# Optimization experiments

Measured on AMD Instinct MI355X. Metric: run time of the kernel, lower is better.

## Reference

```python
import jax, jax.numpy as jnp
import numpy as np

B, N, C = 4, 2048, 81
IMG_W, IMG_H = 1024.0, 800.0
SCORE_THRESH = 0.05
NMS_THRESH = 0.5
DETS_PER_IMG = 100
BBOX_XFORM_CLIP = float(np.log(1000.0 / 16.0))
WX, WY, WW, WH = 10.0, 10.0, 5.0, 5.0


def _make_boxes(key, n):
    k1, k2, k3, k4 = jax.random.split(key, 4)
    x1 = jax.random.uniform(k1, (n,)) * (IMG_W - 60.0)
    y1 = jax.random.uniform(k2, (n,)) * (IMG_H - 60.0)
    w = 10.0 + jax.random.uniform(k3, (n,)) * 300.0
    h = 10.0 + jax.random.uniform(k4, (n,)) * 300.0
    return jnp.stack([x1, y1, jnp.minimum(x1 + w, IMG_W - 1.0), jnp.minimum(y1 + h, IMG_H - 1.0)], axis=-1)


def setup_inputs() -> dict:
    key = jax.random.key(0)
    k1, k2, k3, k4 = jax.random.split(key, 4)
    return {
        "class_logits": jax.random.normal(k1, (B * N, C), jnp.float32),
        "box_regression": jax.random.normal(k2, (B * N, C * 8), jnp.float32) * 0.5,
        "left_proposals": _make_boxes(k3, B * N),
        "right_proposals": _make_boxes(k4, B * N),
    }


def decode(rel, boxes):
    widths = boxes[:, 2] - boxes[:, 0] + 1.0
    heights = boxes[:, 3] - boxes[:, 1] + 1.0
    ctr_x = boxes[:, 0] + 0.5 * widths
    ctr_y = boxes[:, 1] + 0.5 * heights
    dx = rel[:, 0::4] / WX
    dy = rel[:, 1::4] / WY
    dw = jnp.minimum(rel[:, 2::4] / WW, BBOX_XFORM_CLIP)
    dh = jnp.minimum(rel[:, 3::4] / WH, BBOX_XFORM_CLIP)
    pcx = dx * widths[:, None] + ctr_x[:, None]
    pcy = dy * heights[:, None] + ctr_y[:, None]
    pw = jnp.exp(dw) * widths[:, None]
    ph = jnp.exp(dh) * heights[:, None]
    x1 = pcx - 0.5 * pw
    y1 = pcy - 0.5 * ph
    x2 = pcx + 0.5 * pw - 1.0
    y2 = pcy + 0.5 * ph - 1.0
    return jnp.stack([x1, y1, x2, y2], axis=-1)  # [M, C, 4]


def clip_boxes(b):
    x1 = jnp.clip(b[..., 0], 0.0, IMG_W - 1.0)
    y1 = jnp.clip(b[..., 1], 0.0, IMG_H - 1.0)
    x2 = jnp.clip(b[..., 2], 0.0, IMG_W - 1.0)
    y2 = jnp.clip(b[..., 3], 0.0, IMG_H - 1.0)
    return jnp.stack([x1, y1, x2, y2], axis=-1)


def pairwise_iou(b):
    area = jnp.clip(b[:, 2] - b[:, 0] + 1.0, 0.0) * jnp.clip(b[:, 3] - b[:, 1] + 1.0, 0.0)
    lt = jnp.maximum(b[:, None, :2], b[None, :, :2])
    rb = jnp.minimum(b[:, None, 2:], b[None, :, 2:])
    wh = jnp.clip(rb - lt + 1.0, 0.0)
    inter = wh[..., 0] * wh[..., 1]
    return inter / jnp.maximum(area[:, None] + area[None, :] - inter, 1e-6)


def nms_keep(boxes, scores):
    # greedy NMS -> boolean keep mask (fixed shape)
    n = scores.shape[0]
    order = jnp.argsort(-scores)
    iou = pairwise_iou(boxes[order])
    idx = jnp.arange(n)
    def body(i, keep):
        sup = (iou[i] > NMS_THRESH) & keep[i] & (idx > i)
        return keep & (~sup)
    keep = jax.lax.fori_loop(0, n, body, jnp.ones((n,), bool))
    return jnp.zeros((n,), bool).at[order].set(keep)


def _per_image(prob, lb, rb):
    # prob [N,C], lb/rb [N,C,4]
    labels = jnp.argmax(prob, axis=-1)
    ar = jnp.arange(prob.shape[0])
    score = prob[ar, labels]
    lbox = lb[ar, labels]
    rbox = rb[ar, labels]
    valid = (labels >= 1) & (score > SCORE_THRESH)
    s = jnp.where(valid, score, -jnp.inf)
    keep = nms_keep(lbox, s) & nms_keep(rbox, s) & valid
    ms = jnp.where(keep, score, -jnp.inf)
    kth = jax.lax.top_k(ms, DETS_PER_IMG)[0][-1]
    keep = keep & (ms >= kth)
    return lbox, rbox, score, keep


def reference(class_logits, box_regression, left_proposals, right_proposals):
    prob = jax.nn.softmax(class_logits, axis=-1)  # [B*N, C]
    reg = box_regression.reshape(-1, C, 8)
    lb = clip_boxes(decode(reg[:, :, :4].reshape(-1, C * 4), left_proposals))
    rb = clip_boxes(decode(reg[:, :, 4:].reshape(-1, C * 4), right_proposals))
    prob = prob.reshape(B, N, C)
    lb = lb.reshape(B, N, C, 4)
    rb = rb.reshape(B, N, C, 4)
    lbox, rbox, score, keep = jax.vmap(_per_image)(prob, lb, rb)
    m = keep[..., None].astype(score.dtype)
    out = jnp.concatenate([lbox * m, rbox * m, jnp.where(keep, score, 0.0)[..., None]], axis=-1)
    return out  # [B, N, 9]
```

## Files before the change

kernel.cpp:

```cpp
#include <hip/hip_runtime.h>
#include <math.h>

#define NPROP 2048
#define NIMG 4
#define NCLS 81
#define REGW 648
#define SCORE_THRESH 0.05f
#define NMS_T 0.5f
#define DETS 100
#define XC 1023.0f
#define YC 799.0f
#define BBOX_CLIP 4.135166556742356f
#define HBIN 128
#define HOFF 2048
#define SEL 320
#define MAXC 512
#define WRD 8
#define TRIP 2560

typedef unsigned long long u64;

__device__ __forceinline__ float areaf(float4 v) {
  return fmaxf(v.z - v.x + 1.0f, 0.0f) * fmaxf(v.w - v.y + 1.0f, 0.0f);
}
__device__ __forceinline__ bool iou_gt(float4 a, float aa, float4 b, float ba) {
  float ix1 = fmaxf(a.x, b.x), iy1 = fmaxf(a.y, b.y);
  float ix2 = fminf(a.z, b.z), iy2 = fminf(a.w, b.w);
  float iw = fmaxf(ix2 - ix1 + 1.0f, 0.0f);
  float ih = fmaxf(iy2 - iy1 + 1.0f, 0.0f);
  float inter = iw * ih;
  return inter > NMS_T * fmaxf(aa + ba - inter, 1e-6f);
}
__device__ __forceinline__ float score_from_v(unsigned v) {
  unsigned uu = ~v;
  unsigned bits = (uu & 0x80000000u) ? (uu & 0x7fffffffu) : ~uu;
  return __uint_as_float(bits);
}
__device__ __forceinline__ float4 decode_side(const float* __restrict__ reg,
                                              const float4* __restrict__ props,
                                              int grow, int ci, int isR) {
  const float* r = reg + (size_t)grow * REGW + ci * 8 + isR * 4;
  float4 P = props[grow];
  float w  = P.z - P.x + 1.0f;
  float h  = P.w - P.y + 1.0f;
  float cx = P.x + 0.5f * w;
  float cy = P.y + 0.5f * h;
  float dx = r[0] / 10.0f;
  float dy = r[1] / 10.0f;
  float dw = fminf(r[2] / 5.0f, BBOX_CLIP);
  float dh = fminf(r[3] / 5.0f, BBOX_CLIP);
  float pcx = dx * w + cx;
  float pcy = dy * h + cy;
  float pw = expf(dw) * w;
  float ph = expf(dh) * h;
  float4 o;
  o.x = fminf(fmaxf(pcx - 0.5f * pw, 0.0f), XC);
  o.y = fminf(fmaxf(pcy - 0.5f * ph, 0.0f), YC);
  o.z = fminf(fmaxf(pcx + 0.5f * pw - 1.0f, 0.0f), XC);
  o.w = fminf(fmaxf(pcy + 0.5f * ph - 1.0f, 0.0f), YC);
  return o;
}

__global__ __launch_bounds__(256) void score_kernel(
    const float* __restrict__ logits, const float* __restrict__ reg,
    const float* __restrict__ lp, const float* __restrict__ rp,
    unsigned* __restrict__ v32G, unsigned short* __restrict__ ci16G,
    float4* __restrict__ bxAllL, float4* __restrict__ bxAllR,
    int* __restrict__ doneG, float* __restrict__ out) {
  int row  = blockIdx.x * 4 + (threadIdx.x >> 6);
  int lane = threadIdx.x & 63;
  if (blockIdx.x < 72) {
    int g = blockIdx.x * 256 + threadIdx.x;
    ((float4*)out)[g] = make_float4(0.f, 0.f, 0.f, 0.f);
  }
  if (blockIdx.x == 100 && threadIdx.x < NIMG) doneG[threadIdx.x] = 0;
  const float* lr = logits + (size_t)row * NCLS;
  float a = lr[lane];
  float b = (lane < NCLS - 64) ? lr[lane + 64] : -INFINITY;
  float v; int ci;
  if (b > a) { v = b; ci = lane + 64; } else { v = a; ci = lane; }
  for (int o = 32; o; o >>= 1) {
    float ov = __shfl_xor(v, o);
    int   oc = __shfl_xor(ci, o);
    if (ov > v || (ov == v && oc < ci)) { v = ov; ci = oc; }
  }
  float e = expf(a - v) + ((lane < NCLS - 64) ? expf(b - v) : 0.0f);
  for (int o = 32; o; o >>= 1) e += __shfl_xor(e, o);
  if (lane == 0) {
    float score = 1.0f / e;
    unsigned vv = 0xFFFFFFFFu;
    if (ci >= 1 && score > SCORE_THRESH) {
      unsigned uu = __float_as_uint(score);
      uu = (uu & 0x80000000u) ? ~uu : (uu | 0x80000000u);
      vv = ~uu;
    }
    v32G[row]  = vv;
    ci16G[row] = (unsigned short)ci;
    bxAllL[row] = decode_side(reg, (const float4*)lp, row, ci, 0);
    bxAllR[row] = decode_side(reg, (const float4*)rp, row, ci, 1);
  }
}

struct SN {
  u64 keys[NPROP];
  unsigned short sidx[NPROP];
  unsigned v32s[NPROP];
  float4 bxL[MAXC], bxR[MAXC];
  float  arL[MAXC], arR[MAXC];
  u64 keepbL[NPROP / 64], keepbR[NPROP / 64];
  u64 rowmL[64], rowmR[64];
  float4 cbL[64], cbR[64];
  float  cbLa[64], cbRa[64];
  u64 aL, aR;
  int cnt, prevCount, done, ccL, ccR, needFB;
  unsigned kthV;
};

__device__ __forceinline__ float4 get_sboxN(SN* S, const float* reg,
                                            const float4* lp4, const float4* rp4,
                                            const unsigned short* ci16G,
                                            int b, int pos, int isR) {
  if (pos < MAXC) return isR ? S->bxR[pos] : S->bxL[pos];
  int row = S->sidx[pos];
  int grow = b * NPROP + row;
  return decode_side(reg, isR ? rp4 : lp4, grow, ci16G[grow], isR);
}

__global__ __launch_bounds__(1024) void nms_finale_kernel(
    const unsigned* __restrict__ v32G, const unsigned short* __restrict__ ci16G,
    const float* __restrict__ reg, const float* __restrict__ lp,
    const float* __restrict__ rp,
    const float4* __restrict__ bxAllL, const float4* __restrict__ bxAllR,
    unsigned short* __restrict__ srowG, unsigned* __restrict__ svG,
    float4* __restrict__ bxLG, float4* __restrict__ bxRG,
    u64* __restrict__ keepLG, u64* __restrict__ keepRG,
    int* __restrict__ doneG, float* __restrict__ out) {
  __shared__ int hist[HBIN];
  __shared__ u64 keys[MAXC];
  __shared__ unsigned short ssort[MAXC];
  __shared__ float4 bx[MAXC];
  __shared__ u64 mat[TRIP];
  __shared__ int Ts, cnts, nv_sh;
  __shared__ SN S;
  int b = blockIdx.x >> 1, side = blockIdx.x & 1;
  int tid = threadIdx.x, ln = tid & 63, w = tid >> 6;
  const unsigned* v32 = v32G + b * NPROP;
  float* ob = out + (size_t)b * NPROP * 9;

  if (tid == 0) { Ts = HBIN - 1; cnts = 0; }
  if (tid < HBIN) hist[tid] = 0;
  __syncthreads();
  for (int p = tid; p < NPROP; p += 1024) {
    unsigned v = v32[p];
    if (v != 0xFFFFFFFFu) {
      int bin = min(max((int)(v >> 19) - HOFF, 0), HBIN - 1);
      atomicAdd(&hist[bin], 1);
    }
  }
  __syncthreads();
  if (w == 0) {
    int b0 = hist[2 * ln], b1 = hist[2 * ln + 1];
    int s = b0 + b1;
    int incl = s;
#pragma unroll
    for (int o = 1; o < 64; o <<= 1) { int n = __shfl_up(incl, o); if (ln >= o) incl += n; }
    int off = incl - s;
    int c0 = off + b0, c1 = off + s;
    if      (c0 >= SEL && off < SEL) Ts = 2 * ln;
    else if (c1 >= SEL && c0  < SEL) Ts = 2 * ln + 1;
    if (ln == 63) nv_sh = incl;
  }
  __syncthreads();
  int T = Ts, nvTot = nv_sh;
  for (int p = tid; p < NPROP; p += 1024) {
    unsigned v = v32[p];
    bool cand = false;
    if (v != 0xFFFFFFFFu) {
      int bin = min(max((int)(v >> 19) - HOFF, 0), HBIN - 1);
      cand = (bin <= T);
    }
    u64 mb = __ballot(cand);
    int lpos = (int)__popcll(mb & ((1ull << ln) - 1ull));
    int wb = 0;
    if (ln == 0 && mb) wb = atomicAdd(&cnts, (int)__popcll(mb));
    wb = __shfl(wb, 0);
    if (cand) {
      int dst = wb + lpos;
      if (dst < MAXC) keys[dst] = ((u64)v << 16) | (unsigned)p;
    }
  }
  __syncthreads();
  int C1 = cnts;
  bool okfast = (C1 <= MAXC);
  int C1f = okfast ? C1 : 0;

  if (okfast && C1 > 0) {
    if (tid < 256) {
      int i0 = tid, i1 = tid + 256;
      u64 k0 = (i0 < C1) ? keys[i0] : ~0ull;
      u64 k1 = (i1 < C1) ? keys[i1] : ~0ull;
      int r0 = 0, r1 = 0;
#pragma unroll 4
      for (int j = 0; j < C1; ++j) {
        u64 kj = keys[j];
        r0 += (kj < k0) ? 1 : 0;
        r1 += (kj < k1) ? 1 : 0;
      }
      if (i0 < C1) {
        unsigned short rw = (unsigned short)(k0 & 0xFFFFull);
        ssort[r0] = rw; srowG[b * MAXC + r0] = rw;
        svG[b * MAXC + r0] = (unsigned)(k0 >> 16);
      }
      if (i1 < C1) {
        unsigned short rw = (unsigned short)(k1 & 0xFFFFull);
        ssort[r1] = rw; srowG[b * MAXC + r1] = rw;
        svG[b * MAXC + r1] = (unsigned)(k1 >> 16);
      }
    }
    __syncthreads();
    if (tid < MAXC) {
      float4 B = make_float4(0.f, 0.f, 0.f, 0.f);
      if (tid < C1) {
        int row = ssort[tid];
        B = (side ? bxAllR : bxAllL)[b * NPROP + row];
        (side ? bxRG : bxLG)[b * MAXC + tid] = B;
      }
      bx[tid] = B;
    }
    __syncthreads();
    int WRDu = (C1 + 63) >> 6;
    {
      int rb = w & 7, part = w >> 3;
      int r = rb * 64 + ln;
      float4 rbx = bx[r];
      float  rar = areaf(rbx);
      int tb = 0;
      for (int k = 0; k < rb; ++k) tb += ((8 - k) | 1);
      int Sw = (8 - rb) | 1;
      u64* myrow = &mat[tb * 64 + ln * Sw];
      for (int cw = rb + part; cw < WRDu; cw += 2) {
        u64 m = 0;
        const float4* cp = &bx[cw * 64];
#pragma unroll 8
        for (int c = 0; c < 64; ++c) {
          float4 cb = cp[c];
          float car = areaf(cb);
          if (iou_gt(rbx, rar, cb, car)) m |= (1ull << c);
        }
        if (cw == rb) m &= ~((2ull << ln) - 1ull);
        myrow[cw - rb] = m;
      }
    }
    __syncthreads();
    if (w == 0) {
      u64 A[WRD];
#pragma unroll
      for (int t = 0; t < WRD; ++t) {
        int b0 = t * 64;
        A[t] = (C1 >= b0 + 64) ? ~0ull : (C1 > b0 ? ((1ull << (C1 - b0)) - 1ull) : 0ull);
      }
      int tbase = 0;
#pragma unroll
      for (int wb = 0; wb < WRD; ++wb) {
        if (wb * 64 < C1) {
          const int Sw = (8 - wb) | 1;
          const u64* rowp = &mat[tbase];
          u64 aw = A[wb];
#pragma unroll
          for (int g = 0; g < 4; ++g) {
            u64 d[16];
#pragma unroll
            for (int k = 0; k < 16; ++k) d[k] = rowp[(g * 16 + k) * Sw];
#pragma unroll
            for (int k = 0; k < 16; ++k) {
              u64 msk = 0ull - ((aw >> (g * 16 + k)) & 1ull);
              aw &= ~(msk & d[k]);
            }
          }
          A[wb] = aw;
          bool alive = (aw >> ln) & 1ull;
#pragma unroll
          for (int t = wb + 1; t < WRD; ++t) {
            if (t * 64 < C1) {
              u64 x = alive ? rowp[ln * Sw + (t - wb)] : 0ull;
#pragma unroll
              for (int o = 1; o < 64; o <<= 1)
                x |= __shfl_xor((unsigned long long)x, o);
              A[t] &= ~x;
            }
          }
        }
        tbase += 64 * ((8 - wb) | 1);
      }
      if (ln == 0) {
        u64* kG = (side ? keepRG : keepLG) + b * WRD;
#pragma unroll
        for (int t = 0; t < WRD; ++t)
          if (t * 64 < C1) kG[t] = A[t];
      }
    }
  }
  __threadfence();
  __syncthreads();
  if (tid == 0) atomicAdd(doneG + b, 1);
  if (side == 1) return;

  if (tid == 0) {
    while (__hip_atomic_load(doneG + b, __ATOMIC_ACQUIRE, __HIP_MEMORY_SCOPE_AGENT) < 2)
      __builtin_amdgcn_s_sleep(8);
  }
  __syncthreads();
  __threadfence();

  if (w == 0) {
    int before = 0;
    unsigned kth = 0;
    for (int wb = 0; wb * 64 < C1f; ++wb) {
      u64 m = keepLG[b * WRD + wb] & keepRG[b * WRD + wb];
      int pos = wb * 64 + ln;
      bool bit = (m >> ln) & 1ull;
      int rank = before + (int)__popcll(m & ((1ull << ln) - 1ull));
      unsigned vA = svG[b * MAXC + pos];
      u64 selm = __ballot(bit && rank == DETS - 1);
      if (selm) kth = __shfl(vA, __ffsll(selm) - 1);
      bool qual = bit && (rank < DETS || vA == kth);
      if (qual) {
        int row = srowG[b * MAXC + pos];
        float4 L = bxLG[b * MAXC + pos], R = bxRG[b * MAXC + pos];
        float* orow = ob + row * 9;
        orow[0]=L.x; orow[1]=L.y; orow[2]=L.z; orow[3]=L.w;
        orow[4]=R.x; orow[5]=R.y; orow[6]=R.z; orow[7]=R.w;
        orow[8]=score_from_v(vA);
      }
      before += (int)__popcll(m);
    }
    if (ln == 0) {
      S.needFB = (before < DETS && nvTot > C1f) ? 1 : 0;
      S.cnt = 0; S.prevCount = 0; S.done = 0; S.kthV = 0u;
    }
  }
  __syncthreads();
  if (!S.needFB) return;

  const float4* lp4 = (const float4*)lp;
  const float4* rp4 = (const float4*)rp;
  float4* ob4 = (float4*)ob;
  float4 z4 = make_float4(0.f, 0.f, 0.f, 0.f);
  for (int i = tid; i < NPROP * 9 / 4; i += 1024) ob4[i] = z4;
  for (int p = tid; p < NPROP; p += 1024) {
    unsigned v = v32G[b * NPROP + p];
    S.v32s[p] = v;
    bool cand = (v != 0xFFFFFFFFu);
    u64 mb = __ballot(cand);
    int lpos = (int)__popcll(mb & ((1ull << ln) - 1ull));
    int wb = 0;
    if (ln == 0 && mb) wb = atomicAdd(&S.cnt, (int)__popcll(mb));
    wb = __shfl(wb, 0);
    if (cand) S.keys[wb + lpos] = ((u64)v << 16) | (unsigned)p;
  }
  __syncthreads();
  int C2 = S.cnt;
  int CbEnd = (C2 + 63) & ~63;
  {
    int i0 = tid, i1 = tid + 1024;
    u64 k0 = (i0 < C2) ? S.keys[i0] : ~0ull;
    u64 k1 = (i1 < C2) ? S.keys[i1] : ~0ull;
    int r0 = 0, r1 = 0;
#pragma unroll 4
    for (int j = 0; j < C2; ++j) {
      u64 kj = S.keys[j];
      r0 += (kj < k0) ? 1 : 0;
      r1 += (kj < k1) ? 1 : 0;
    }
    if (i0 < C2) S.sidx[r0] = (unsigned short)(k0 & 0xFFFFull);
    if (i1 < C2) S.sidx[r1] = (unsigned short)(k1 & 0xFFFFull);
  }
  for (int i = C2 + tid; i < CbEnd; i += 1024) S.sidx[i] = 0;
  for (int wd = tid; wd < NPROP / 64; wd += 1024) {
    int b0 = wd << 6;
    u64 mf = 0ull;
    if (C2 >= b0 + 64) mf = ~0ull;
    else if (C2 > b0)  mf = (1ull << (C2 - b0)) - 1ull;
    S.keepbL[wd] = mf; S.keepbR[wd] = mf;
  }
  __syncthreads();
  {
    int lim = min(CbEnd, MAXC);
    for (int i = tid; i < lim; i += 1024) {
      if (i < C2) {
        int row = S.sidx[i];
        int grow = b * NPROP + row;
        int ci = ci16G[grow];
        float4 L = decode_side(reg, lp4, grow, ci, 0);
        float4 R = decode_side(reg, rp4, grow, ci, 1);
        S.bxL[i] = L; S.arL[i] = areaf(L);
        S.bxR[i] = R; S.arR[i] = areaf(R);
      } else {
        S.bxL[i] = z4; S.arL[i] = 1.0f;
        S.bxR[i] = z4; S.arR[i] = 1.0f;
      }
    }
  }
  __syncthreads();
  for (int base = 0; base < CbEnd; base += 64) {
    {
      int isR = (w >= 8);
      float4 cbx = get_sboxN(&S, reg, lp4, rp4, ci16G, b, base + ln, isR);
      float car = (base + ln < MAXC) ? (isR ? S.arR[base + ln] : S.arL[base + ln])
                                     : areaf(cbx);
      int w8 = w & 7;
#pragma unroll
      for (int k = 0; k < 8; ++k) {
        int row = w8 * 8 + k;
        float4 rbx;
        rbx.x = __shfl(cbx.x, row); rbx.y = __shfl(cbx.y, row);
        rbx.z = __shfl(cbx.z, row); rbx.w = __shfl(cbx.w, row);
        float rar = __shfl(car, row);
        bool bit = (ln > row) && iou_gt(rbx, rar, cbx, car);
        u64 bal = __ballot(bit);
        if (ln == 0) { if (isR) S.rowmR[row] = bal; else S.rowmL[row] = bal; }
      }
    }
    __syncthreads();
    if (tid < 128) {
      int isR = (tid >= 64);
      u64* km = isR ? S.keepbR : S.keepbL;
      u64* rm = isR ? S.rowmR  : S.rowmL;
      u64 a = km[base >> 6];
#pragma unroll
      for (int j = 0; j < 64; ++j)
        a &= ~((0ull - ((a >> j) & 1ull)) & rm[j]);
      if (ln == 0) {
        km[base >> 6] = a;
        if (isR) { S.aR = a; S.ccR = __popcll(a); }
        else     { S.aL = a; S.ccL = __popcll(a); }
      }
      if ((a >> ln) & 1ull) {
        int pos = __popcll(a & ((1ull << ln) - 1ull));
        float4 v = get_sboxN(&S, reg, lp4, rp4, ci16G, b, base + ln, isR);
        if (isR) { S.cbR[pos] = v; S.cbRa[pos] = areaf(v); }
        else     { S.cbL[pos] = v; S.cbLa[pos] = areaf(v); }
      }
    }
    __syncthreads();
    if (w == 0) {
      u64 m = S.aL & S.aR;
      int before = S.prevCount;
      bool bit = (m >> ln) & 1ull;
      int rank = before + (int)__popcll(m & ((1ull << ln) - 1ull));
      int row = S.sidx[base + ln];
      unsigned vA = S.v32s[row];
      u64 selm = __ballot(bit && rank == DETS - 1);
      unsigned keffV = S.kthV;
      if (selm) keffV = __shfl(vA, __ffsll(selm) - 1);
      bool qual = bit && (rank < DETS || vA == keffV);
      if (qual) {
        float4 L = get_sboxN(&S, reg, lp4, rp4, ci16G, b, base + ln, 0);
        float4 R = get_sboxN(&S, reg, lp4, rp4, ci16G, b, base + ln, 1);
        float s = score_from_v(vA);
        float* orow = ob + row * 9;
        orow[0]=L.x; orow[1]=L.y; orow[2]=L.z; orow[3]=L.w;
        orow[4]=R.x; orow[5]=R.y; orow[6]=R.z; orow[7]=R.w;
        orow[8]=s;
      }
      if (ln == 0) {
        if (selm) S.kthV = keffV;
        int nc = before + (int)__popcll(m);
        S.prevCount = nc;
        if (nc >= DETS) {
          int nxt = base + 64;
          bool cont = false;
          if (nxt < C2) cont = (S.v32s[S.sidx[nxt]] == keffV);
          if (!cont) S.done = 1;
        }
      }
    } else {
      int cL = S.ccL, cR = S.ccR;
      if ((cL | cR) != 0) {
        for (int p = base + 64 + (tid - 64); p < CbEnd; p += 960) {
          float4 mbL = get_sboxN(&S, reg, lp4, rp4, ci16G, b, p, 0);
          float al = (p < MAXC) ? S.arL[p] : areaf(mbL);
          bool supL = false;
          for (int q = 0; q < cL; ++q)
            supL = supL || iou_gt(mbL, al, S.cbL[q], S.cbLa[q]);
          if (supL) atomicAnd(&S.keepbL[p >> 6], ~(1ull << (p & 63)));
          float4 mbR = get_sboxN(&S, reg, lp4, rp4, ci16G, b, p, 1);
          float ar_ = (p < MAXC) ? S.arR[p] : areaf(mbR);
          bool supR = false;
          for (int q = 0; q < cR; ++q)
            supR = supR || iou_gt(mbR, ar_, S.cbR[q], S.cbRa[q]);
          if (supR) atomicAnd(&S.keepbR[p >> 6], ~(1ull << (p & 63)));
        }
      }
    }
    __syncthreads();
    if (S.done) break;
  }
}

extern "C" void kernel_launch(void* const* d_in, const int* in_sizes, int n_in,
                              void* d_out, int out_size, void* d_ws, size_t ws_size,
                              hipStream_t stream) {
  const float* logits = (const float*)d_in[0];
  const float* reg    = (const float*)d_in[1];
  const float* lprop  = (const float*)d_in[2];
  const float* rprop  = (const float*)d_in[3];
  float* out = (float*)d_out;

  char* ws = (char*)d_ws;
  unsigned*       v32G   = (unsigned*)(ws + 0);
  unsigned short* ci16G  = (unsigned short*)(ws + 32768);
  unsigned short* srowG  = (unsigned short*)(ws + 49152);
  unsigned*       svG    = (unsigned*)(ws + 53248);
  float4*         bxLG   = (float4*)(ws + 61440);
  float4*         bxRG   = (float4*)(ws + 94208);
  u64*            keepLG = (u64*)(ws + 126976);
  u64*            keepRG = (u64*)(ws + 127232);
  int*            doneG  = (int*)(ws + 127488);
  float4*         bxAllL = (float4*)(ws + 131072);
  float4*         bxAllR = (float4*)(ws + 262144);

  score_kernel<<<NIMG * NPROP / 4, 256,  0, stream>>>(logits, reg, lprop, rprop,
                                                      v32G, ci16G, bxAllL, bxAllR,
                                                      doneG, out);
  nms_finale_kernel<<<2 * NIMG,    1024, 0, stream>>>(v32G, ci16G, reg, lprop, rprop,
                                                      bxAllL, bxAllR, srowG, svG,
                                                      bxLG, bxRG, keepLG, keepRG,
                                                      doneG, out);
}
```

Baseline: 128.5 us.

## Split fused NMS/finale kernel into separate launches instead of spin-wait

Replaces the single NMS+finale kernel, which used a global done-counter with a spin-wait between the left and right side blocks, with two kernels. One runs the per-side NMS and writes counts and flags, the other does the merge, the output writes and the fallback. This removes the inter-block busy-wait and its threadfence, and it also removes the side-1 blocks idling. The cost is one extra kernel launch and a pass of metadata through global memory.

```diff
diff --git a/kernel.cpp b/kernel.cpp
--- a/kernel.cpp
+++ b/kernel.cpp
@@ -66,14 +66,13 @@
     const float* __restrict__ lp, const float* __restrict__ rp,
     unsigned* __restrict__ v32G, unsigned short* __restrict__ ci16G,
     float4* __restrict__ bxAllL, float4* __restrict__ bxAllR,
-    int* __restrict__ doneG, float* __restrict__ out) {
+    float* __restrict__ out) {
   int row  = blockIdx.x * 4 + (threadIdx.x >> 6);
   int lane = threadIdx.x & 63;
   if (blockIdx.x < 72) {
     int g = blockIdx.x * 256 + threadIdx.x;
     ((float4*)out)[g] = make_float4(0.f, 0.f, 0.f, 0.f);
   }
-  if (blockIdx.x == 100 && threadIdx.x < NIMG) doneG[threadIdx.x] = 0;
   const float* lr = logits + (size_t)row * NCLS;
   float a = lr[lane];
   float b = (lane < NCLS - 64) ? lr[lane + 64] : -INFINITY;
@@ -98,6 +97,182 @@
     ci16G[row] = (unsigned short)ci;
     bxAllL[row] = decode_side(reg, (const float4*)lp, row, ci, 0);
     bxAllR[row] = decode_side(reg, (const float4*)rp, row, ci, 1);
+  }
+}
+
+__global__ __launch_bounds__(1024) void nms8_kernel(
+    const unsigned* __restrict__ v32G,
+    const float4* __restrict__ bxAllL, const float4* __restrict__ bxAllR,
+    unsigned short* __restrict__ srowG, unsigned* __restrict__ svG,
+    float4* __restrict__ bxLG, float4* __restrict__ bxRG,
+    u64* __restrict__ keepLG, u64* __restrict__ keepRG,
+    int* __restrict__ C1G, int* __restrict__ C2G, int* __restrict__ flagG) {
+  __shared__ int hist[HBIN];
+  __shared__ u64 keys[MAXC];
+  __shared__ unsigned short ssort[MAXC];
+  __shared__ float4 bx[MAXC];
+  __shared__ u64 mat[TRIP];
+  __shared__ int Ts, cnts, nv_sh;
+  int b = blockIdx.x >> 1, side = blockIdx.x & 1;
+  int tid = threadIdx.x, ln = tid & 63, w = tid >> 6;
+  const unsigned* v32 = v32G + b * NPROP;
+
+  if (tid == 0) { Ts = HBIN - 1; cnts = 0; }
+  if (tid < HBIN) hist[tid] = 0;
+  __syncthreads();
+  for (int p = tid; p < NPROP; p += 1024) {
+    unsigned v = v32[p];
+    if (v != 0xFFFFFFFFu) {
+      int bin = min(max((int)(v >> 19) - HOFF, 0), HBIN - 1);
+      atomicAdd(&hist[bin], 1);
+    }
+  }
+  __syncthreads();
+  if (w == 0) {
+    int b0 = hist[2 * ln], b1 = hist[2 * ln + 1];
+    int s = b0 + b1;
+    int incl = s;
+#pragma unroll
+    for (int o = 1; o < 64; o <<= 1) { int n = __shfl_up(incl, o); if (ln >= o) incl += n; }
+    int off = incl - s;
+    int c0 = off + b0, c1 = off + s;
+    if      (c0 >= SEL && off < SEL) Ts = 2 * ln;
+    else if (c1 >= SEL && c0  < SEL) Ts = 2 * ln + 1;
+    if (ln == 63) nv_sh = incl;
+  }
+  __syncthreads();
+  int T = Ts, nvTot = nv_sh;
+  for (int p = tid; p < NPROP; p += 1024) {
+    unsigned v = v32[p];
+    bool cand = false;
+    if (v != 0xFFFFFFFFu) {
+      int bin = min(max((int)(v >> 19) - HOFF, 0), HBIN - 1);
+      cand = (bin <= T);
+    }
+    u64 mb = __ballot(cand);
+    int lpos = (int)__popcll(mb & ((1ull << ln) - 1ull));
+    int wb = 0;
+    if (ln == 0 && mb) wb = atomicAdd(&cnts, (int)__popcll(mb));
+    wb = __shfl(wb, 0);
+    if (cand) {
+      int dst = wb + lpos;
+      if (dst < MAXC) keys[dst] = ((u64)v << 16) | (unsigned)p;
+    }
+  }
+  __syncthreads();
+  int C1 = cnts;
+  if (C1 > MAXC) {
+    if (tid == 0) { flagG[b] = 1; C1G[b] = 0; C2G[b] = nvTot; }
+    return;
+  }
+  if (tid == 0) { flagG[b] = 0; C1G[b] = C1; C2G[b] = nvTot; }
+  if (C1 == 0) return;
+
+  if (tid < 256) {
+    int i0 = tid, i1 = tid + 256;
+    u64 k0 = (i0 < C1) ? keys[i0] : ~0ull;
+    u64 k1 = (i1 < C1) ? keys[i1] : ~0ull;
+    int r0 = 0, r1 = 0;
+#pragma unroll 4
+    for (int j = 0; j < C1; ++j) {
+      u64 kj = keys[j];
+      r0 += (kj < k0) ? 1 : 0;
+      r1 += (kj < k1) ? 1 : 0;
+    }
+    if (i0 < C1) {
+      unsigned short rw = (unsigned short)(k0 & 0xFFFFull);
+      ssort[r0] = rw; srowG[b * MAXC + r0] = rw;
+      svG[b * MAXC + r0] = (unsigned)(k0 >> 16);
+    }
+    if (i1 < C1) {
+      unsigned short rw = (unsigned short)(k1 & 0xFFFFull);
+      ssort[r1] = rw; srowG[b * MAXC + r1] = rw;
+      svG[b * MAXC + r1] = (unsigned)(k1 >> 16);
+    }
+  }
+  __syncthreads();
+  if (tid < MAXC) {
+    float4 B = make_float4(0.f, 0.f, 0.f, 0.f);
+    if (tid < C1) {
+      int row = ssort[tid];
+      B = (side ? bxAllR : bxAllL)[b * NPROP + row];
+      (side ? bxRG : bxLG)[b * MAXC + tid] = B;
+    }
+    bx[tid] = B;
+  }
+  __syncthreads();
+
+  int WRDu = (C1 + 63) >> 6;
+  {
+    int rb = w & 7, part = w >> 3;
+    int r = rb * 64 + ln;
+    float4 rbx = bx[r];
+    float  rar = areaf(rbx);
+    int tb = 0;
+    for (int k = 0; k < rb; ++k) tb += ((8 - k) | 1);
+    int Sw = (8 - rb) | 1;
+    u64* myrow = &mat[tb * 64 + ln * Sw];
+    for (int cw = rb + part; cw < WRDu; cw += 2) {
+      u64 m = 0;
+      const float4* cp = &bx[cw * 64];
+#pragma unroll 8
+      for (int c = 0; c < 64; ++c) {
+        float4 cb = cp[c];
+        float car = areaf(cb);
+        if (iou_gt(rbx, rar, cb, car)) m |= (1ull << c);
+      }
+      if (cw == rb) m &= ~((2ull << ln) - 1ull);
+      myrow[cw - rb] = m;
+    }
+  }
+  __syncthreads();
+
+  if (w == 0) {
+    u64 A[WRD];
+#pragma unroll
+    for (int t = 0; t < WRD; ++t) {
+      int b0 = t * 64;
+      A[t] = (C1 >= b0 + 64) ? ~0ull : (C1 > b0 ? ((1ull << (C1 - b0)) - 1ull) : 0ull);
+    }
+    int tbase = 0;
+#pragma unroll
+    for (int wb = 0; wb < WRD; ++wb) {
+      if (wb * 64 < C1) {
+        const int Sw = (8 - wb) | 1;
+        const u64* rowp = &mat[tbase];
+        u64 aw = A[wb];
+#pragma unroll
+        for (int g = 0; g < 4; ++g) {
+          u64 d[16];
+#pragma unroll
+          for (int k = 0; k < 16; ++k) d[k] = rowp[(g * 16 + k) * Sw];
+#pragma unroll
+          for (int k = 0; k < 16; ++k) {
+            u64 msk = 0ull - ((aw >> (g * 16 + k)) & 1ull);
+            aw &= ~(msk & d[k]);
+          }
+        }
+        A[wb] = aw;
+        bool alive = (aw >> ln) & 1ull;
+#pragma unroll
+        for (int t = wb + 1; t < WRD; ++t) {
+          if (t * 64 < C1) {
+            u64 x = alive ? rowp[ln * Sw + (t - wb)] : 0ull;
+#pragma unroll
+            for (int o = 1; o < 64; o <<= 1)
+              x |= __shfl_xor((unsigned long long)x, o);
+            A[t] &= ~x;
+          }
+        }
+      }
+      tbase += 64 * ((8 - wb) | 1);
+    }
+    if (ln == 0) {
+      u64* kG = (side ? keepRG : keepLG) + b * WRD;
+#pragma unroll
+      for (int t = 0; t < WRD; ++t)
+        if (t * 64 < C1) kG[t] = A[t];
+    }
   }
 }
 
@@ -126,196 +301,24 @@
   return decode_side(reg, isR ? rp4 : lp4, grow, ci16G[grow], isR);
 }
 
-__global__ __launch_bounds__(1024) void nms_finale_kernel(
-    const unsigned* __restrict__ v32G, const unsigned short* __restrict__ ci16G,
+__global__ __launch_bounds__(1024) void finale_fallback_kernel(
     const float* __restrict__ reg, const float* __restrict__ lp,
-    const float* __restrict__ rp,
-    const float4* __restrict__ bxAllL, const float4* __restrict__ bxAllR,
-    unsigned short* __restrict__ srowG, unsigned* __restrict__ svG,
-    float4* __restrict__ bxLG, float4* __restrict__ bxRG,
-    u64* __restrict__ keepLG, u64* __restrict__ keepRG,
-    int* __restrict__ doneG, float* __restrict__ out) {
-  __shared__ int hist[HBIN];
-  __shared__ u64 keys[MAXC];
-  __shared__ unsigned short ssort[MAXC];
-  __shared__ float4 bx[MAXC];
-  __shared__ u64 mat[TRIP];
-  __shared__ int Ts, cnts, nv_sh;
+    const float* __restrict__ rp, const unsigned* __restrict__ v32G,
+    const unsigned short* __restrict__ ci16G,
+    const u64* __restrict__ keepLG, const u64* __restrict__ keepRG,
+    const unsigned* __restrict__ svG, const unsigned short* __restrict__ srowG,
+    const float4* __restrict__ bxLG, const float4* __restrict__ bxRG,
+    const int* __restrict__ C1G, const int* __restrict__ C2G,
+    const int* __restrict__ flagG, float* __restrict__ out) {
   __shared__ SN S;
-  int b = blockIdx.x >> 1, side = blockIdx.x & 1;
-  int tid = threadIdx.x, ln = tid & 63, w = tid >> 6;
-  const unsigned* v32 = v32G + b * NPROP;
+  int b = blockIdx.x, tid = threadIdx.x, ln = tid & 63, w = tid >> 6;
   float* ob = out + (size_t)b * NPROP * 9;
 
-  if (tid == 0) { Ts = HBIN - 1; cnts = 0; }
-  if (tid < HBIN) hist[tid] = 0;
-  __syncthreads();
-  for (int p = tid; p < NPROP; p += 1024) {
-    unsigned v = v32[p];
-    if (v != 0xFFFFFFFFu) {
-      int bin = min(max((int)(v >> 19) - HOFF, 0), HBIN - 1);
-      atomicAdd(&hist[bin], 1);
-    }
-  }
-  __syncthreads();
   if (w == 0) {
-    int b0 = hist[2 * ln], b1 = hist[2 * ln + 1];
-    int s = b0 + b1;
-    int incl = s;
-#pragma unroll
-    for (int o = 1; o < 64; o <<= 1) { int n = __shfl_up(incl, o); if (ln >= o) incl += n; }
-    int off = incl - s;
-    int c0 = off + b0, c1 = off + s;
-    if      (c0 >= SEL && off < SEL) Ts = 2 * ln;
-    else if (c1 >= SEL && c0  < SEL) Ts = 2 * ln + 1;
-    if (ln == 63) nv_sh = incl;
-  }
-  __syncthreads();
-  int T = Ts, nvTot = nv_sh;
-  for (int p = tid; p < NPROP; p += 1024) {
-    unsigned v = v32[p];
-    bool cand = false;
-    if (v != 0xFFFFFFFFu) {
-      int bin = min(max((int)(v >> 19) - HOFF, 0), HBIN - 1);
-      cand = (bin <= T);
-    }
-    u64 mb = __ballot(cand);
-    int lpos = (int)__popcll(mb & ((1ull << ln) - 1ull));
-    int wb = 0;
-    if (ln == 0 && mb) wb = atomicAdd(&cnts, (int)__popcll(mb));
-    wb = __shfl(wb, 0);
-    if (cand) {
-      int dst = wb + lpos;
-      if (dst < MAXC) keys[dst] = ((u64)v << 16) | (unsigned)p;
-    }
-  }
-  __syncthreads();
-  int C1 = cnts;
-  bool okfast = (C1 <= MAXC);
-  int C1f = okfast ? C1 : 0;
-
-  if (okfast && C1 > 0) {
-    if (tid < 256) {
-      int i0 = tid, i1 = tid + 256;
-      u64 k0 = (i0 < C1) ? keys[i0] : ~0ull;
-      u64 k1 = (i1 < C1) ? keys[i1] : ~0ull;
-      int r0 = 0, r1 = 0;
-#pragma unroll 4
-      for (int j = 0; j < C1; ++j) {
-        u64 kj = keys[j];
-        r0 += (kj < k0) ? 1 : 0;
-        r1 += (kj < k1) ? 1 : 0;
-      }
-      if (i0 < C1) {
-        unsigned short rw = (unsigned short)(k0 & 0xFFFFull);
-        ssort[r0] = rw; srowG[b * MAXC + r0] = rw;
-        svG[b * MAXC + r0] = (unsigned)(k0 >> 16);
-      }
-      if (i1 < C1) {
-        unsigned short rw = (unsigned short)(k1 & 0xFFFFull);
-        ssort[r1] = rw; srowG[b * MAXC + r1] = rw;
-        svG[b * MAXC + r1] = (unsigned)(k1 >> 16);
-      }
-    }
-    __syncthreads();
-    if (tid < MAXC) {
-      float4 B = make_float4(0.f, 0.f, 0.f, 0.f);
-      if (tid < C1) {
-        int row = ssort[tid];
-        B = (side ? bxAllR : bxAllL)[b * NPROP + row];
-        (side ? bxRG : bxLG)[b * MAXC + tid] = B;
-      }
-      bx[tid] = B;
-    }
-    __syncthreads();
-    int WRDu = (C1 + 63) >> 6;
-    {
-      int rb = w & 7, part = w >> 3;
-      int r = rb * 64 + ln;
-      float4 rbx = bx[r];
-      float  rar = areaf(rbx);
-      int tb = 0;
-      for (int k = 0; k < rb; ++k) tb += ((8 - k) | 1);
-      int Sw = (8 - rb) | 1;
-      u64* myrow = &mat[tb * 64 + ln * Sw];
-      for (int cw = rb + part; cw < WRDu; cw += 2) {
-        u64 m = 0;
-        const float4* cp = &bx[cw * 64];
-#pragma unroll 8
-        for (int c = 0; c < 64; ++c) {
-          float4 cb = cp[c];
-          float car = areaf(cb);
-          if (iou_gt(rbx, rar, cb, car)) m |= (1ull << c);
-        }
-        if (cw == rb) m &= ~((2ull << ln) - 1ull);
-        myrow[cw - rb] = m;
-      }
-    }
-    __syncthreads();
-    if (w == 0) {
-      u64 A[WRD];
-#pragma unroll
-      for (int t = 0; t < WRD; ++t) {
-        int b0 = t * 64;
-        A[t] = (C1 >= b0 + 64) ? ~0ull : (C1 > b0 ? ((1ull << (C1 - b0)) - 1ull) : 0ull);
-      }
-      int tbase = 0;
-#pragma unroll
-      for (int wb = 0; wb < WRD; ++wb) {
-        if (wb * 64 < C1) {
-          const int Sw = (8 - wb) | 1;
-          const u64* rowp = &mat[tbase];
-          u64 aw = A[wb];
-#pragma unroll
-          for (int g = 0; g < 4; ++g) {
-            u64 d[16];
-#pragma unroll
-            for (int k = 0; k < 16; ++k) d[k] = rowp[(g * 16 + k) * Sw];
-#pragma unroll
-            for (int k = 0; k < 16; ++k) {
-              u64 msk = 0ull - ((aw >> (g * 16 + k)) & 1ull);
-              aw &= ~(msk & d[k]);
-            }
-          }
-          A[wb] = aw;
-          bool alive = (aw >> ln) & 1ull;
-#pragma unroll
-          for (int t = wb + 1; t < WRD; ++t) {
-            if (t * 64 < C1) {
-              u64 x = alive ? rowp[ln * Sw + (t - wb)] : 0ull;
-#pragma unroll
-              for (int o = 1; o < 64; o <<= 1)
-                x |= __shfl_xor((unsigned long long)x, o);
-              A[t] &= ~x;
-            }
-          }
-        }
-        tbase += 64 * ((8 - wb) | 1);
-      }
-      if (ln == 0) {
-        u64* kG = (side ? keepRG : keepLG) + b * WRD;
-#pragma unroll
-        for (int t = 0; t < WRD; ++t)
-          if (t * 64 < C1) kG[t] = A[t];
-      }
-    }
-  }
-  __threadfence();
-  __syncthreads();
-  if (tid == 0) atomicAdd(doneG + b, 1);
-  if (side == 1) return;
-
-  if (tid == 0) {
-    while (__hip_atomic_load(doneG + b, __ATOMIC_ACQUIRE, __HIP_MEMORY_SCOPE_AGENT) < 2)
-      __builtin_amdgcn_s_sleep(8);
-  }
-  __syncthreads();
-  __threadfence();
-
-  if (w == 0) {
+    int C1 = C1G[b];
     int before = 0;
     unsigned kth = 0;
-    for (int wb = 0; wb * 64 < C1f; ++wb) {
+    for (int wb = 0; wb * 64 < C1; ++wb) {
       u64 m = keepLG[b * WRD + wb] & keepRG[b * WRD + wb];
       int pos = wb * 64 + ln;
       bool bit = (m >> ln) & 1ull;
@@ -335,7 +338,7 @@
       before += (int)__popcll(m);
     }
     if (ln == 0) {
-      S.needFB = (before < DETS && nvTot > C1f) ? 1 : 0;
+      S.needFB = ((before < DETS && C2G[b] > C1) || flagG[b]) ? 1 : 0;
       S.cnt = 0; S.prevCount = 0; S.done = 0; S.kthV = 0u;
     }
   }
@@ -516,15 +519,18 @@
   float4*         bxRG   = (float4*)(ws + 94208);
   u64*            keepLG = (u64*)(ws + 126976);
   u64*            keepRG = (u64*)(ws + 127232);
-  int*            doneG  = (int*)(ws + 127488);
+  int*            C1G    = (int*)(ws + 127488);
+  int*            C2G    = (int*)(ws + 127504);
+  int*            flagG  = (int*)(ws + 127520);
   float4*         bxAllL = (float4*)(ws + 131072);
   float4*         bxAllR = (float4*)(ws + 262144);
 
   score_kernel<<<NIMG * NPROP / 4, 256,  0, stream>>>(logits, reg, lprop, rprop,
-                                                      v32G, ci16G, bxAllL, bxAllR,
-                                                      doneG, out);
-  nms_finale_kernel<<<2 * NIMG,    1024, 0, stream>>>(v32G, ci16G, reg, lprop, rprop,
-                                                      bxAllL, bxAllR, srowG, svG,
-                                                      bxLG, bxRG, keepLG, keepRG,
-                                                      doneG, out);
-}
+                                                      v32G, ci16G, bxAllL, bxAllR, out);
+  nms8_kernel <<<2 * NIMG,         1024, 0, stream>>>(v32G, bxAllL, bxAllR,
+                                                      srowG, svG, bxLG, bxRG,
+                                                      keepLG, keepRG, C1G, C2G, flagG);
+  finale_fallback_kernel<<<NIMG,   1024, 0, stream>>>(reg, lprop, rprop, v32G, ci16G,
+                                                      keepLG, keepRG, svG, srowG,
+                                                      bxLG, bxRG, C1G, C2G, flagG, out);
+}
```

New measurement: 124.5 us. 3.1% less time.
